# Performance work log

Hardware: AMD Instinct MI355X
Metric: run time of the kernel (lower is better)

The kernel has to match this reference:

```python
import jax, jax.numpy as jnp
import numpy as np

N_NODES = 50000
N_EDGES = 800000
IN_CH = 128
OUT_CH = 128
TIME_DIM = 64


def setup_inputs() -> dict:
    key = jax.random.key(0)
    ks = jax.random.split(key, 7)
    x = jax.random.normal(ks[0], (N_NODES, IN_CH), dtype=jnp.float32)
    edge_index = jax.random.randint(ks[1], (2, N_EDGES), 0, N_NODES, dtype=jnp.int64)
    edge_t = jax.random.uniform(ks[2], (N_EDGES,), dtype=jnp.float32)
    # parameters
    freqs = jax.random.normal(ks[3], (TIME_DIM // 2,), dtype=jnp.float32)
    fan = IN_CH + TIME_DIM
    lim = float(np.sqrt(1.0 / fan))
    lin_w = jax.random.uniform(ks[4], (OUT_CH, fan), minval=-lim, maxval=lim, dtype=jnp.float32)
    lin_b = jax.random.uniform(ks[5], (OUT_CH,), minval=-lim, maxval=lim, dtype=jnp.float32)
    glim = float(np.sqrt(6.0 / (1 + OUT_CH)))
    attn = jax.random.uniform(ks[6], (1, OUT_CH), minval=-glim, maxval=glim, dtype=jnp.float32)
    return {"x": x, "edge_index": edge_index, "edge_t": edge_t,
            "freqs": freqs, "lin_w": lin_w, "lin_b": lin_b, "attn": attn}


def reference(x, edge_index, edge_t, freqs, lin_w, lin_b, attn):
    src, dst = edge_index[0], edge_index[1]
    n_nodes = x.shape[0]
    # time encoding: [E, time_dim]
    ang = edge_t[:, None] * freqs * (2.0 * jnp.pi)
    edge_attr = jnp.concatenate([jnp.sin(ang), jnp.cos(ang)], axis=-1)
    # gather source features and project: h = tanh(Linear(cat(x_j, te)))
    msg = jnp.concatenate([x[src], edge_attr], axis=-1)        # [E, in+time]
    h = jnp.tanh(msg @ lin_w.T + lin_b)                        # [E, out]
    # segment softmax over destination nodes
    alpha = (h * attn).sum(axis=-1)                            # [E]
    seg_max = jax.ops.segment_max(alpha, dst, num_segments=n_nodes)
    ex = jnp.exp(alpha - seg_max[dst])
    denom = jax.ops.segment_sum(ex, dst, num_segments=n_nodes)
    w = ex / (denom[dst] + 1e-16)
    # scatter-add aggregation
    out = jax.ops.segment_sum(h * w[:, None], dst, num_segments=n_nodes)
    return out
```

## Files before the change

### kernel.cpp

```cpp
#include <hip/hip_runtime.h>
#include <hip/hip_bf16.h>
#include <math.h>

#define IN_CHN 128
#define OUT_CHN 128
#define KD 192
#define TM 64

typedef __bf16 bf16x8 __attribute__((ext_vector_type(8)));
typedef float f32x4 __attribute__((ext_vector_type(4)));

static __device__ __forceinline__ unsigned short f2b(float f) {
    return __builtin_bit_cast(unsigned short, (__bf16)f);
}
static __device__ __forceinline__ float b2f(unsigned short b) {
    return __uint_as_float(((unsigned int)b) << 16);
}
static __device__ __forceinline__ float fast_tanh(float x) {
    float e = __expf(2.0f * x);
    return 1.0f - 2.0f * __builtin_amdgcn_rcpf(e + 1.0f);
}

#define GLL16(gsrc, ldst) \
    __builtin_amdgcn_global_load_lds( \
        (const __attribute__((address_space(1))) unsigned int*)(gsrc), \
        (__attribute__((address_space(3))) unsigned int*)(ldst), 16, 0, 0)


__global__ __launch_bounds__(256) void cvt_x(const float* __restrict__ x,
    unsigned short* __restrict__ xb, long long n8)
{
    long long i = (long long)blockIdx.x * 256 + threadIdx.x;
    if (i >= n8) return;
    const float4* src = (const float4*)(x + i * 8);
    float4 v0 = src[0], v1 = src[1];
    ushort4 p0 = { f2b(v0.x), f2b(v0.y), f2b(v0.z), f2b(v0.w) };
    ushort4 p1 = { f2b(v1.x), f2b(v1.y), f2b(v1.z), f2b(v1.w) };
    *(ushort4*)(xb + i * 8)     = p0;
    *(ushort4*)(xb + i * 8 + 4) = p1;
}


__global__ __launch_bounds__(256) void count_deg(const int* __restrict__ ei,
                                                 int* __restrict__ deg, int E) {
    int e = blockIdx.x * 256 + threadIdx.x;
    if (e < E) atomicAdd(&deg[ei[E + e]], 1);
}

static __device__ __forceinline__ int wave_incl_scan(int v, int lane) {
    #pragma unroll
    for (int off = 1; off < 64; off <<= 1) {
        int t = __shfl_up(v, off);
        if (lane >= off) v += t;
    }
    return v;
}

__global__ __launch_bounds__(256) void scan_local(const int* __restrict__ deg,
    int* __restrict__ offs, int* __restrict__ partial, int Nn)
{
    __shared__ int wsum[4];
    int tid = threadIdx.x, lane = tid & 63, wid = tid >> 6;
    int i = blockIdx.x * 256 + tid;
    int v = (i < Nn) ? deg[i] : 0;
    int incl = wave_incl_scan(v, lane);
    if (lane == 63) wsum[wid] = incl;
    __syncthreads();
    int wpre = 0;
    for (int w = 0; w < wid; ++w) wpre += wsum[w];
    if (i < Nn) offs[i] = wpre + incl - v;
    if (tid == 255) partial[blockIdx.x] = wpre + incl;
}

__global__ __launch_bounds__(256) void scan_partial(int* __restrict__ partial, int nparts)
{
    __shared__ int wsum[4];
    int tid = threadIdx.x, lane = tid & 63, wid = tid >> 6;
    int v = (tid < nparts) ? partial[tid] : 0;
    int incl = wave_incl_scan(v, lane);
    if (lane == 63) wsum[wid] = incl;
    __syncthreads();
    int wpre = 0;
    for (int w = 0; w < wid; ++w) wpre += wsum[w];
    if (tid < nparts) partial[tid] = wpre + incl - v;
}

__global__ __launch_bounds__(256) void finalize_offs(int* __restrict__ offs,
    const int* __restrict__ partial, int* __restrict__ cursor, int Nn)
{
    int i = blockIdx.x * 256 + threadIdx.x;
    if (i < Nn) { int o = offs[i] + partial[i >> 8]; offs[i] = o; cursor[i] = o; }
}

__global__ __launch_bounds__(256) void fill_perm(const int* __restrict__ ei,
    const float* __restrict__ et, int* __restrict__ cursor,
    uint2* __restrict__ mt, int E)
{
    int e = blockIdx.x * 256 + threadIdx.x;
    if (e < E) {
        int d = ei[E + e];
        int pos = atomicAdd(&cursor[d], 1);
        mt[pos] = make_uint2((unsigned)ei[e], __float_as_uint(et[e]));
    }
}


__device__ __forceinline__ void load_meta(const uint2* __restrict__ mt,
    int tile, int E, int wv, int g, int lane, int sv[4], float& tsv)
{
    int e0 = tile * TM;
    #pragma unroll
    for (int i = 0; i < 4; ++i) {
        int e = e0 + wv * 16 + i * 4 + g;
        sv[i] = (int)mt[e < E ? e : E - 1].x;
    }
    int el = e0 + lane;
    tsv = __uint_as_float(mt[el < E ? el : E - 1].y);
}

__global__ __launch_bounds__(256) void gemm_mfma(
    const unsigned short* __restrict__ xb, const uint2* __restrict__ mt,
    const float* __restrict__ freqs, const float* __restrict__ lw,
    const float* __restrict__ lb, const float* __restrict__ attn,
    unsigned short* __restrict__ h_p, float* __restrict__ alpha_p,
    int E, int n_tiles)
{
    __shared__ unsigned short xs[2][TM][128];
    __shared__ unsigned short te[2][TM * 64];
    __shared__ float apart[2][4][TM];

    const int tid  = threadIdx.x;
    const int lane = tid & 63;
    const int wv   = tid >> 6;
    const int c16  = lane & 15;
    const int g    = lane >> 4;
    const int wbase = wv * 32;
    const int sgr  = lane & 7;

    bf16x8 Wf[6][2];
    #pragma unroll
    for (int kk = 0; kk < 6; ++kk)
        #pragma unroll
        for (int nf = 0; nf < 2; ++nf) {
            const float* wp = lw + (size_t)(wbase + nf * 16 + c16) * KD + kk * 32 + g * 8;
            float4 v0 = *(const float4*)wp;
            float4 v1 = *(const float4*)(wp + 4);
            bf16x8 b;
            b[0] = (__bf16)v0.x; b[1] = (__bf16)v0.y; b[2] = (__bf16)v0.z; b[3] = (__bf16)v0.w;
            b[4] = (__bf16)v1.x; b[5] = (__bf16)v1.y; b[6] = (__bf16)v1.z; b[7] = (__bf16)v1.w;
            Wf[kk][nf] = b;
        }

    f32x4 bias_v[2], attn_v[2];
    #pragma unroll
    for (int nf = 0; nf < 2; ++nf) {
        bias_v[nf] = *(const f32x4*)(lb   + wbase + nf * 16 + g * 4);
        attn_v[nf] = *(const f32x4*)(attn + wbase + nf * 16 + g * 4);
    }

    float frv[8];
    #pragma unroll
    for (int j = 0; j < 8; ++j) frv[j] = freqs[wv * 8 + j] * 6.283185307179586f;

    const int stride = gridDim.x;
    float ts_cur, ts_nxt;
    int sv_nxt[4];

    {
        int sv0[4];
        load_meta(mt, blockIdx.x, E, wv, g, lane, sv0, ts_cur);
        #pragma unroll
        for (int i = 0; i < 4; ++i) {
            const int rlo = i * 4 + g;
            const unsigned short* gsrc = xb + (size_t)sv0[i] * IN_CHN + ((c16 ^ rlo) * 8);
            GLL16(gsrc, &xs[0][wv * 16 + i * 4][0]);
        }
        int t1 = blockIdx.x + stride;
        load_meta(mt, t1 < n_tiles ? t1 : n_tiles - 1, E, wv, g, lane, sv_nxt, ts_nxt);
    }

    int cur = 0;
    int prev_e0 = -1;

    for (int tile = blockIdx.x; tile < n_tiles; tile += stride) {
        const int e0 = tile * TM;

        int sv2[4]; float ts2;
        {
            int t2 = tile + 2 * stride;
            load_meta(mt, t2 < n_tiles ? t2 : n_tiles - 1, E, wv, g, lane, sv2, ts2);
        }

        {
            float sj[8], cj[8];
            #pragma unroll
            for (int j = 0; j < 8; ++j) {
                float ang = ts_cur * frv[j];
                sj[j] = __sinf(ang);
                cj[j] = __cosf(ang);
            }
            unsigned short* tr = &te[cur][lane * 64];
            int gs = (wv ^ sgr) * 8;
            int gc = ((wv + 4) ^ sgr) * 8;
            *(ushort4*)(tr + gs)     = (ushort4){ f2b(sj[0]), f2b(sj[1]), f2b(sj[2]), f2b(sj[3]) };
            *(ushort4*)(tr + gs + 4) = (ushort4){ f2b(sj[4]), f2b(sj[5]), f2b(sj[6]), f2b(sj[7]) };
            *(ushort4*)(tr + gc)     = (ushort4){ f2b(cj[0]), f2b(cj[1]), f2b(cj[2]), f2b(cj[3]) };
            *(ushort4*)(tr + gc + 4) = (ushort4){ f2b(cj[4]), f2b(cj[5]), f2b(cj[6]), f2b(cj[7]) };
        }

        __syncthreads();

        if (tile + stride < n_tiles) {
            #pragma unroll
            for (int i = 0; i < 4; ++i) {
                const int rlo = i * 4 + g;
                const unsigned short* gsrc = xb + (size_t)sv_nxt[i] * IN_CHN + ((c16 ^ rlo) * 8);
                GLL16(gsrc, &xs[cur ^ 1][wv * 16 + i * 4][0]);
            }
        }

        if (prev_e0 >= 0 && tid < TM) {
            int e = prev_e0 + tid;
            if (e < E)
                alpha_p[e] = apart[cur ^ 1][0][tid] + apart[cur ^ 1][1][tid]
                           + apart[cur ^ 1][2][tid] + apart[cur ^ 1][3][tid];
        }

        f32x4 acc[4][2];
        #pragma unroll
        for (int mi = 0; mi < 4; ++mi) {
            acc[mi][0] = (f32x4){0.f, 0.f, 0.f, 0.f};
            acc[mi][1] = (f32x4){0.f, 0.f, 0.f, 0.f};
        }

        const unsigned short* xsc = &xs[cur][0][0];
        const unsigned short* tec = &te[cur][0];
        #pragma unroll
        for (int mi = 0; mi < 4; ++mi) {
            const int r = mi * 16 + c16;
            const unsigned short* xrow = xsc + r * 128;
            #pragma unroll
            for (int kk = 0; kk < 4; ++kk) {
                const int slot = ((kk << 2) + g) ^ c16;
                bf16x8 a = __builtin_bit_cast(bf16x8, *(const uint4*)(xrow + slot * 8));
                acc[mi][0] = __builtin_amdgcn_mfma_f32_16x16x32_bf16(Wf[kk][0], a, acc[mi][0], 0, 0, 0);
                acc[mi][1] = __builtin_amdgcn_mfma_f32_16x16x32_bf16(Wf[kk][1], a, acc[mi][1], 0, 0, 0);
            }
            const unsigned short* trow = tec + r * 64;
            bf16x8 s8 = __builtin_bit_cast(bf16x8, *(const uint4*)(trow + ((g ^ (r & 7)) * 8)));
            bf16x8 c8 = __builtin_bit_cast(bf16x8, *(const uint4*)(trow + (((g + 4) ^ (r & 7)) * 8)));
            acc[mi][0] = __builtin_amdgcn_mfma_f32_16x16x32_bf16(Wf[4][0], s8, acc[mi][0], 0, 0, 0);
            acc[mi][1] = __builtin_amdgcn_mfma_f32_16x16x32_bf16(Wf[4][1], s8, acc[mi][1], 0, 0, 0);
            acc[mi][0] = __builtin_amdgcn_mfma_f32_16x16x32_bf16(Wf[5][0], c8, acc[mi][0], 0, 0, 0);
            acc[mi][1] = __builtin_amdgcn_mfma_f32_16x16x32_bf16(Wf[5][1], c8, acc[mi][1], 0, 0, 0);
        }

        #pragma unroll
        for (int mi = 0; mi < 4; ++mi) {
            int e = e0 + mi * 16 + c16;
            float p = 0.0f;
            ushort4 pv[2];
            #pragma unroll
            for (int nf = 0; nf < 2; ++nf) {
                f32x4 z = acc[mi][nf];
                #pragma unroll
                for (int r = 0; r < 4; ++r) {
                    float h = fast_tanh(z[r] + bias_v[nf][r]);
                    z[r] = h;
                    p = fmaf(h, attn_v[nf][r], p);
                }
                pv[nf] = (ushort4){ f2b(z[0]), f2b(z[1]), f2b(z[2]), f2b(z[3]) };
            }
            p += __shfl_xor(p, 16);
            p += __shfl_xor(p, 32);
            if (e < E) {
                unsigned short* hp = h_p + (size_t)e * OUT_CHN + wbase + g * 4;
                *(ushort4*)hp        = pv[0];
                *(ushort4*)(hp + 16) = pv[1];
            }
            if (g == 0) apart[cur][wv][mi * 16 + c16] = p;
        }

        prev_e0 = e0;
        ts_cur = ts_nxt; ts_nxt = ts2;
        #pragma unroll
        for (int i = 0; i < 4; ++i) sv_nxt[i] = sv2[i];
        cur ^= 1;
    }

    __syncthreads();
    if (prev_e0 >= 0 && tid < TM) {
        int e = prev_e0 + tid;
        if (e < E)
            alpha_p[e] = apart[cur ^ 1][0][tid] + apart[cur ^ 1][1][tid]
                       + apart[cur ^ 1][2][tid] + apart[cur ^ 1][3][tid];
    }
}


__global__ __launch_bounds__(256) void agg(
    const unsigned short* __restrict__ h_p, const float* __restrict__ alpha_p,
    const int* __restrict__ offs, const int* __restrict__ deg,
    float* __restrict__ out, int Nn)
{
    int wid  = threadIdx.x >> 6;
    int lane = threadIdx.x & 63;
    int node = blockIdx.x * 4 + wid;
    if (node >= Nn) return;
    int start = offs[node];
    int d = deg[node];
    int sub = lane >> 4;
    int ch  = (lane & 15) * 8;
    float4* op = (float4*)(out + (size_t)node * OUT_CHN + ch);
    if (d == 0) {
        if (sub == 0) { op[0] = (float4){0,0,0,0}; op[1] = (float4){0,0,0,0}; }
        return;
    }

    float m = -INFINITY;
    for (int i = lane; i < d; i += 64) m = fmaxf(m, alpha_p[start + i]);
    #pragma unroll
    for (int off = 32; off > 0; off >>= 1) m = fmaxf(m, __shfl_xor(m, off));

    float s = 0.0f;
    for (int i = lane; i < d; i += 64) s += __expf(alpha_p[start + i] - m);
    #pragma unroll
    for (int off = 32; off > 0; off >>= 1) s += __shfl_xor(s, off);
    float rs = __builtin_amdgcn_rcpf(s + 1e-16f);

    float a[8];
    #pragma unroll
    for (int q = 0; q < 8; ++q) a[q] = 0.0f;

    for (int i = 0; i < d; i += 4) {
        int idx = i + sub;
        float w = 0.0f;
        uint4 hv = {0u, 0u, 0u, 0u};
        if (idx < d) {
            w = __expf(alpha_p[start + idx] - m) * rs;
            hv = *(const uint4*)(h_p + (size_t)(start + idx) * OUT_CHN + ch);
        }
        unsigned int hw[4] = { hv.x, hv.y, hv.z, hv.w };
        #pragma unroll
        for (int q = 0; q < 4; ++q) {
            a[2*q]   = fmaf(b2f((unsigned short)(hw[q] & 0xFFFFu)), w, a[2*q]);
            a[2*q+1] = fmaf(b2f((unsigned short)(hw[q] >> 16)),     w, a[2*q+1]);
        }
    }
    #pragma unroll
    for (int q = 0; q < 8; ++q) {
        a[q] += __shfl_xor(a[q], 16);
        a[q] += __shfl_xor(a[q], 32);
    }
    if (sub == 0) {
        op[0] = (float4){a[0], a[1], a[2], a[3]};
        op[1] = (float4){a[4], a[5], a[6], a[7]};
    }
}


extern "C" void kernel_launch(void* const* d_in, const int* in_sizes, int n_in,
                              void* d_out, int out_size, void* d_ws, size_t ws_size,
                              hipStream_t stream) {
    const float* x     = (const float*)d_in[0];
    const int*   ei    = (const int*)d_in[1];
    const float* et    = (const float*)d_in[2];
    const float* freqs = (const float*)d_in[3];
    const float* lw    = (const float*)d_in[4];
    const float* lb    = (const float*)d_in[5];
    const float* attn  = (const float*)d_in[6];
    float* out = (float*)d_out;

    const int E  = in_sizes[2];
    const int Nn = in_sizes[0] / IN_CHN;

    char* ws = (char*)d_ws;
    unsigned short* h_p = (unsigned short*)ws;
    size_t off = (size_t)E * OUT_CHN * sizeof(unsigned short);
    float* alpha_p = (float*)(ws + off); off += (size_t)E * sizeof(float);
    uint2* mt      = (uint2*)(ws + off); off += (size_t)E * sizeof(uint2);
    unsigned short* xb = (unsigned short*)(ws + off); off += (size_t)Nn * IN_CHN * sizeof(unsigned short);
    int*   deg     = (int*)(ws + off);   off += (size_t)Nn * sizeof(int);
    int*   offs    = (int*)(ws + off);   off += (size_t)Nn * sizeof(int);
    int*   cursor  = (int*)(ws + off);   off += (size_t)Nn * sizeof(int);
    int*   partial = (int*)(ws + off);

    const int nblk = (Nn + 255) / 256;
    const int eblk = (E + 255) / 256;

    long long n8 = (long long)Nn * IN_CHN / 8;
    cvt_x<<<(unsigned)((n8 + 255) / 256), 256, 0, stream>>>(x, xb, n8);

    hipMemsetAsync(deg, 0, (size_t)Nn * sizeof(int), stream);
    count_deg<<<eblk, 256, 0, stream>>>(ei, deg, E);
    scan_local<<<nblk, 256, 0, stream>>>(deg, offs, partial, Nn);
    scan_partial<<<1, 256, 0, stream>>>(partial, nblk);
    finalize_offs<<<nblk, 256, 0, stream>>>(offs, partial, cursor, Nn);
    fill_perm<<<eblk, 256, 0, stream>>>(ei, et, cursor, mt, E);

    const int n_tiles = (E + TM - 1) / TM;
    gemm_mfma<<<768, 256, 0, stream>>>(xb, mt, freqs, lw, lb, attn,
                                       h_p, alpha_p, E, n_tiles);

    agg<<<(Nn + 3) / 4, 256, 0, stream>>>(h_p, alpha_p, offs, deg, out, Nn);
}
```

Before: 267.1 us.

## Single-buffer time encoding, write alpha partials to global, add reduce kernel

The GEMM kernel now keeps the time-encoding tile in a single LDS buffer. The sin/cos values are computed into registers before the barrier and stored to LDS after it, followed by a second lightweight LDS barrier. The cross-wave alpha reduction through LDS (apart) is removed: each wave writes its partial dot product to a per-wave global array, and a new sum_alpha kernel adds the four partials. The grid grows from 768 to 1024 blocks, likely for occupancy from the reduced LDS. This adds an extra kernel launch, extra global traffic for the alpha partials, and a second barrier per tile.

After: 250.8 us. -6.1%, faster.

```diff
diff --git a/kernel.cpp b/kernel.cpp
--- a/kernel.cpp
+++ b/kernel.cpp
@@ -25,6 +25,12 @@
     __builtin_amdgcn_global_load_lds( \
         (const __attribute__((address_space(1))) unsigned int*)(gsrc), \
         (__attribute__((address_space(3))) unsigned int*)(ldst), 16, 0, 0)
+
+#define LDS_BARRIER() do { \
+    asm volatile("s_waitcnt lgkmcnt(0)" ::: "memory"); \
+    __builtin_amdgcn_s_barrier(); \
+    __builtin_amdgcn_sched_barrier(0); \
+} while (0)
 
 
 __global__ __launch_bounds__(256) void cvt_x(const float* __restrict__ x,
@@ -122,12 +128,11 @@
     const unsigned short* __restrict__ xb, const uint2* __restrict__ mt,
     const float* __restrict__ freqs, const float* __restrict__ lw,
     const float* __restrict__ lb, const float* __restrict__ attn,
-    unsigned short* __restrict__ h_p, float* __restrict__ alpha_p,
-    int E, int n_tiles)
+    unsigned short* __restrict__ h_p, float* __restrict__ alpha4,
+    int E, int Ep, int n_tiles)
 {
     __shared__ unsigned short xs[2][TM][128];
-    __shared__ unsigned short te[2][TM * 64];
-    __shared__ float apart[2][4][TM];
+    __shared__ unsigned short te[TM * 64];
 
     const int tid  = threadIdx.x;
     const int lane = tid & 63;
@@ -180,17 +185,11 @@
     }
 
     int cur = 0;
-    int prev_e0 = -1;
 
     for (int tile = blockIdx.x; tile < n_tiles; tile += stride) {
         const int e0 = tile * TM;
 
-        int sv2[4]; float ts2;
-        {
-            int t2 = tile + 2 * stride;
-            load_meta(mt, t2 < n_tiles ? t2 : n_tiles - 1, E, wv, g, lane, sv2, ts2);
-        }
-
+        ushort4 tp[4];
         {
             float sj[8], cj[8];
             #pragma unroll
@@ -199,13 +198,16 @@
                 sj[j] = __sinf(ang);
                 cj[j] = __cosf(ang);
             }
-            unsigned short* tr = &te[cur][lane * 64];
-            int gs = (wv ^ sgr) * 8;
-            int gc = ((wv + 4) ^ sgr) * 8;
-            *(ushort4*)(tr + gs)     = (ushort4){ f2b(sj[0]), f2b(sj[1]), f2b(sj[2]), f2b(sj[3]) };
-            *(ushort4*)(tr + gs + 4) = (ushort4){ f2b(sj[4]), f2b(sj[5]), f2b(sj[6]), f2b(sj[7]) };
-            *(ushort4*)(tr + gc)     = (ushort4){ f2b(cj[0]), f2b(cj[1]), f2b(cj[2]), f2b(cj[3]) };
-            *(ushort4*)(tr + gc + 4) = (ushort4){ f2b(cj[4]), f2b(cj[5]), f2b(cj[6]), f2b(cj[7]) };
+            tp[0] = (ushort4){ f2b(sj[0]), f2b(sj[1]), f2b(sj[2]), f2b(sj[3]) };
+            tp[1] = (ushort4){ f2b(sj[4]), f2b(sj[5]), f2b(sj[6]), f2b(sj[7]) };
+            tp[2] = (ushort4){ f2b(cj[0]), f2b(cj[1]), f2b(cj[2]), f2b(cj[3]) };
+            tp[3] = (ushort4){ f2b(cj[4]), f2b(cj[5]), f2b(cj[6]), f2b(cj[7]) };
+        }
+
+        int sv2[4]; float ts2;
+        {
+            int t2 = tile + 2 * stride;
+            load_meta(mt, t2 < n_tiles ? t2 : n_tiles - 1, E, wv, g, lane, sv2, ts2);
         }
 
         __syncthreads();
@@ -219,12 +221,17 @@
             }
         }
 
-        if (prev_e0 >= 0 && tid < TM) {
-            int e = prev_e0 + tid;
-            if (e < E)
-                alpha_p[e] = apart[cur ^ 1][0][tid] + apart[cur ^ 1][1][tid]
-                           + apart[cur ^ 1][2][tid] + apart[cur ^ 1][3][tid];
-        }
+        {
+            unsigned short* tr = &te[lane * 64];
+            int gs = (wv ^ sgr) * 8;
+            int gc = ((wv + 4) ^ sgr) * 8;
+            *(ushort4*)(tr + gs)     = tp[0];
+            *(ushort4*)(tr + gs + 4) = tp[1];
+            *(ushort4*)(tr + gc)     = tp[2];
+            *(ushort4*)(tr + gc + 4) = tp[3];
+        }
+
+        LDS_BARRIER();
 
         f32x4 acc[4][2];
         #pragma unroll
@@ -234,7 +241,6 @@
         }
 
         const unsigned short* xsc = &xs[cur][0][0];
-        const unsigned short* tec = &te[cur][0];
         #pragma unroll
         for (int mi = 0; mi < 4; ++mi) {
             const int r = mi * 16 + c16;
@@ -246,7 +252,7 @@
                 acc[mi][0] = __builtin_amdgcn_mfma_f32_16x16x32_bf16(Wf[kk][0], a, acc[mi][0], 0, 0, 0);
                 acc[mi][1] = __builtin_amdgcn_mfma_f32_16x16x32_bf16(Wf[kk][1], a, acc[mi][1], 0, 0, 0);
             }
-            const unsigned short* trow = tec + r * 64;
+            const unsigned short* trow = &te[r * 64];
             bf16x8 s8 = __builtin_bit_cast(bf16x8, *(const uint4*)(trow + ((g ^ (r & 7)) * 8)));
             bf16x8 c8 = __builtin_bit_cast(bf16x8, *(const uint4*)(trow + (((g + 4) ^ (r & 7)) * 8)));
             acc[mi][0] = __builtin_amdgcn_mfma_f32_16x16x32_bf16(Wf[4][0], s8, acc[mi][0], 0, 0, 0);
@@ -277,23 +283,34 @@
                 unsigned short* hp = h_p + (size_t)e * OUT_CHN + wbase + g * 4;
                 *(ushort4*)hp        = pv[0];
                 *(ushort4*)(hp + 16) = pv[1];
+                if (g == 0) alpha4[(size_t)wv * Ep + e] = p;
             }
-            if (g == 0) apart[cur][wv][mi * 16 + c16] = p;
-        }
-
-        prev_e0 = e0;
+        }
+
         ts_cur = ts_nxt; ts_nxt = ts2;
         #pragma unroll
         for (int i = 0; i < 4; ++i) sv_nxt[i] = sv2[i];
         cur ^= 1;
     }
-
-    __syncthreads();
-    if (prev_e0 >= 0 && tid < TM) {
-        int e = prev_e0 + tid;
-        if (e < E)
-            alpha_p[e] = apart[cur ^ 1][0][tid] + apart[cur ^ 1][1][tid]
-                       + apart[cur ^ 1][2][tid] + apart[cur ^ 1][3][tid];
+}
+
+
+__global__ __launch_bounds__(256) void sum_alpha(const float* __restrict__ a4,
+    float* __restrict__ ap, int E, int Ep)
+{
+    int i = blockIdx.x * 256 + threadIdx.x;
+    int e = i * 4;
+    if (e + 3 < E) {
+        float4 v0 = *(const float4*)(a4 + e);
+        float4 v1 = *(const float4*)(a4 + Ep + e);
+        float4 v2 = *(const float4*)(a4 + 2 * (size_t)Ep + e);
+        float4 v3 = *(const float4*)(a4 + 3 * (size_t)Ep + e);
+        float4 r = { v0.x + v1.x + v2.x + v3.x, v0.y + v1.y + v2.y + v3.y,
+                     v0.z + v1.z + v2.z + v3.z, v0.w + v1.w + v2.w + v3.w };
+        *(float4*)(ap + e) = r;
+    } else {
+        for (int q = e; q < E; ++q)
+            ap[q] = a4[q] + a4[Ep + q] + a4[2 * (size_t)Ep + q] + a4[3 * (size_t)Ep + q];
     }
 }
 
@@ -373,11 +390,13 @@
 
     const int E  = in_sizes[2];
     const int Nn = in_sizes[0] / IN_CHN;
+    const int Ep = (E + 3) & ~3;
 
     char* ws = (char*)d_ws;
     unsigned short* h_p = (unsigned short*)ws;
     size_t off = (size_t)E * OUT_CHN * sizeof(unsigned short);
-    float* alpha_p = (float*)(ws + off); off += (size_t)E * sizeof(float);
+    float* alpha_p = (float*)(ws + off); off += (size_t)Ep * sizeof(float);
+    float* alpha4  = (float*)(ws + off); off += (size_t)Ep * 4 * sizeof(float);
     uint2* mt      = (uint2*)(ws + off); off += (size_t)E * sizeof(uint2);
     unsigned short* xb = (unsigned short*)(ws + off); off += (size_t)Nn * IN_CHN * sizeof(unsigned short);
     int*   deg     = (int*)(ws + off);   off += (size_t)Nn * sizeof(int);
@@ -399,8 +418,10 @@
     fill_perm<<<eblk, 256, 0, stream>>>(ei, et, cursor, mt, E);
 
     const int n_tiles = (E + TM - 1) / TM;
-    gemm_mfma<<<768, 256, 0, stream>>>(xb, mt, freqs, lw, lb, attn,
-                                       h_p, alpha_p, E, n_tiles);
+    gemm_mfma<<<1024, 256, 0, stream>>>(xb, mt, freqs, lw, lb, attn,
+                                        h_p, alpha4, E, Ep, n_tiles);
+
+    sum_alpha<<<(Ep / 4 + 255) / 256, 256, 0, stream>>>(alpha4, alpha_p, E, Ep);
 
     agg<<<(Nn + 3) / 4, 256, 0, stream>>>(h_p, alpha_p, offs, deg, out, Nn);
 }
```
